# Optimization experiments

Measured on AMD Instinct MI355X. Metric: run time of the kernel, lower is better.

## Reference

```python
import jax, jax.numpy as jnp
import numpy as np

# Sampled-neighborhood sizes (NeighborSampler-style shrinking hops)
N0, N1, N2, N3 = 200000, 50000, 12500, 3200
E0, E1, E2 = 500000, 125000, 32000
D_IN, D_H, D_OUT = 128, 256, 128


def setup_inputs() -> dict:
    key = jax.random.key(0)
    ks = jax.random.split(key, 16)
    x = jax.random.normal(ks[0], (N0, D_IN), dtype=jnp.float32)
    src0 = jax.random.randint(ks[1], (E0,), 0, N0)
    dst0 = jax.random.randint(ks[2], (E0,), 0, N1)
    src1 = jax.random.randint(ks[3], (E1,), 0, N1)
    dst1 = jax.random.randint(ks[4], (E1,), 0, N2)
    src2 = jax.random.randint(ks[5], (E2,), 0, N2)
    dst2 = jax.random.randint(ks[6], (E2,), 0, N3)
    s = 0.05
    # SAGEConv params: lin_l (applied to aggregated neighbors, has bias), lin_r (root)
    wl0 = jax.random.normal(ks[7], (D_H, D_IN), dtype=jnp.float32) * s
    wr0 = jax.random.normal(ks[8], (D_H, D_IN), dtype=jnp.float32) * s
    b0 = jnp.zeros((D_H,), dtype=jnp.float32)
    wl1 = jax.random.normal(ks[9], (D_H, D_H), dtype=jnp.float32) * s
    wr1 = jax.random.normal(ks[10], (D_H, D_H), dtype=jnp.float32) * s
    b1 = jnp.zeros((D_H,), dtype=jnp.float32)
    wl2 = jax.random.normal(ks[11], (D_OUT, D_H), dtype=jnp.float32) * s
    wr2 = jax.random.normal(ks[12], (D_OUT, D_H), dtype=jnp.float32) * s
    b2 = jnp.zeros((D_OUT,), dtype=jnp.float32)
    return {"x": x, "src0": src0, "dst0": dst0, "src1": src1, "dst1": dst1,
            "src2": src2, "dst2": dst2,
            "wl0": wl0, "wr0": wr0, "b0": b0,
            "wl1": wl1, "wr1": wr1, "b1": b1,
            "wl2": wl2, "wr2": wr2, "b2": b2}


def _sage(x, src, dst, n_tgt, wl, wr, b):
    """Bipartite SAGEConv with mean aggregation (PyG default)."""
    x_tgt = x[:n_tgt]                                   # [n_tgt, d_in]
    msg = x[src]                                        # [E, d_in] gather
    s = jax.ops.segment_sum(msg, dst, num_segments=n_tgt)
    cnt = jax.ops.segment_sum(jnp.ones((src.shape[0], 1), x.dtype), dst,
                              num_segments=n_tgt)
    mean = s / jnp.maximum(cnt, 1.0)                    # mean over in-neighbors
    return mean @ wl.T + b + x_tgt @ wr.T               # [n_tgt, d_out]


def reference(x, src0, dst0, src1, dst1, src2, dst2,
              wl0, wr0, b0, wl1, wr1, b1, wl2, wr2, b2):
    h = jax.nn.relu(_sage(x, src0, dst0, N1, wl0, wr0, b0))
    h = jax.nn.relu(_sage(h, src1, dst1, N2, wl1, wr1, b1))
    return _sage(h, src2, dst2, N3, wl2, wr2, b2)       # [N3, D_OUT]
```

## Files before the change

### kernel.cpp

```cpp
#include <hip/hip_runtime.h>

#define N0s 200000
#define N1s 50000
#define N2s 12500
#define N3s 3200
#define E0s 500000
#define E1s 125000
#define E2s 32000
#define D_INs 128
#define D_Hs 256
#define D_OUTs 128

#define CAP 64
#define LOGCAP 6

#define GSTRIDE 72
#define CSTRIDE 132

#define XN4 (N0s * D_INs / 4)
#define WN4 65536
#define CAST_TOTAL (XN4 + WN4)
#define CAST_BLOCKS ((CAST_TOTAL + 2047) / 2048)

typedef __attribute__((ext_vector_type(8))) short short8;
typedef __attribute__((ext_vector_type(4))) float floatx4;

__device__ __forceinline__ unsigned short f32_to_bf16_rne(float f) {
    unsigned int u = __float_as_uint(f);
    u += 0x7fffu + ((u >> 16) & 1u);
    return (unsigned short)(u >> 16);
}
__device__ __forceinline__ float bf16_to_f32(unsigned short h) {
    return __uint_as_float(((unsigned int)h) << 16);
}

struct CastArgs {
    const float* x; unsigned short* xb;
    const float* ws_[6]; unsigned short* wd[6];
};

__launch_bounds__(256)
__global__ void cast_all(CastArgs a)
{
    #pragma unroll
    for (int j = 0; j < 8; ++j) {
        int i = blockIdx.x * 2048 + j * 256 + threadIdx.x;
        if (i < XN4) {
            float4 v = *(const float4*)&a.x[(size_t)i * 4];
            ushort4 o;
            o.x = f32_to_bf16_rne(v.x);
            o.y = f32_to_bf16_rne(v.y);
            o.z = f32_to_bf16_rne(v.z);
            o.w = f32_to_bf16_rne(v.w);
            *(ushort4*)&a.xb[(size_t)i * 4] = o;
        } else if (i < CAST_TOTAL) {
            int g = i - XN4;
            int seg, base;
            if      (g < 8192)  { seg = 0; base = 0; }
            else if (g < 16384) { seg = 1; base = 8192; }
            else if (g < 32768) { seg = 2; base = 16384; }
            else if (g < 49152) { seg = 3; base = 32768; }
            else if (g < 57344) { seg = 4; base = 49152; }
            else                { seg = 5; base = 57344; }
            int k = g - base;
            float4 v = *(const float4*)&a.ws_[seg][(size_t)k * 4];
            ushort4 o;
            o.x = f32_to_bf16_rne(v.x);
            o.y = f32_to_bf16_rne(v.y);
            o.z = f32_to_bf16_rne(v.z);
            o.w = f32_to_bf16_rne(v.w);
            *(ushort4*)&a.wd[seg][(size_t)k * 4] = o;
        }
    }
}

struct Bins {
    const int *src0, *dst0, *src1, *dst1, *src2, *dst2;
    int *cnt0, *cnt1, *cnt2;
    int *eidx0, *eidx1, *eidx2;
};

__launch_bounds__(256)
__global__ void fill3(Bins b)
{
    int e = blockIdx.x * 256 + threadIdx.x;
    if (e < E0s) {
        int d = b.dst0[e];
        int p = atomicAdd(&b.cnt0[d], 1);
        if (p < CAP) b.eidx0[(d << LOGCAP) + p] = b.src0[e];
    } else if (e < E0s + E1s) {
        int i = e - E0s;
        int d = b.dst1[i];
        int p = atomicAdd(&b.cnt1[d], 1);
        if (p < CAP) b.eidx1[(d << LOGCAP) + p] = b.src1[i];
    } else if (e < E0s + E1s + E2s) {
        int i = e - E0s - E1s;
        int d = b.dst2[i];
        int p = atomicAdd(&b.cnt2[d], 1);
        if (p < CAP) b.eidx2[(d << LOGCAP) + p] = b.src2[i];
    }
}

__launch_bounds__(256)
__global__ void gather_mean(const unsigned short* __restrict__ X,
                            const int* __restrict__ eidx,
                            const int* __restrict__ cnt,
                            unsigned short* __restrict__ out,
                            int n_tgt, int D, int logTpr)
{
    int gid = blockIdx.x * 256 + threadIdx.x;
    int row = gid >> logTpr;
    if (row >= n_tgt) return;
    int c = (gid & ((1 << logTpr) - 1)) << 2;

    int deg = cnt[row];
    int e = min(deg, CAP);
    const int* bp = &eidx[row << LOGCAP];

    float a0 = 0.f, a1 = 0.f, a2 = 0.f, a3 = 0.f;
    int i = 0;
    for (; i + 2 <= e; i += 2) {
        int s0 = bp[i], s1 = bp[i + 1];
        ushort4 v0 = *(const ushort4*)&X[(size_t)s0 * D + c];
        ushort4 v1 = *(const ushort4*)&X[(size_t)s1 * D + c];
        a0 += bf16_to_f32(v0.x) + bf16_to_f32(v1.x);
        a1 += bf16_to_f32(v0.y) + bf16_to_f32(v1.y);
        a2 += bf16_to_f32(v0.z) + bf16_to_f32(v1.z);
        a3 += bf16_to_f32(v0.w) + bf16_to_f32(v1.w);
    }
    if (i < e) {
        ushort4 v0 = *(const ushort4*)&X[(size_t)bp[i] * D + c];
        a0 += bf16_to_f32(v0.x); a1 += bf16_to_f32(v0.y);
        a2 += bf16_to_f32(v0.z); a3 += bf16_to_f32(v0.w);
    }
    float inv = 1.0f / fmaxf((float)deg, 1.0f);
    ushort4 o;
    o.x = f32_to_bf16_rne(a0 * inv);
    o.y = f32_to_bf16_rne(a1 * inv);
    o.z = f32_to_bf16_rne(a2 * inv);
    o.w = f32_to_bf16_rne(a3 * inv);
    *(ushort4*)&out[(size_t)row * D + c] = o;
}

__launch_bounds__(256)
__global__ void mfma_gemm(const unsigned short* __restrict__ A1,
                          const unsigned short* __restrict__ A2,
                          const unsigned short* __restrict__ W1,
                          const unsigned short* __restrict__ W2,
                          const float* __restrict__ bias,
                          void* __restrict__ Cout,
                          int M, int N, int K1, int K2,
                          int relu, int out_bf16)
{
    __shared__ unsigned short smem[2 * 128 * GSTRIDE];
    unsigned short* As = smem;
    unsigned short* Bs = smem + 128 * GSTRIDE;

    const int tid  = threadIdx.x;
    const int wave = tid >> 6;
    const int lane = tid & 63;
    const int quad = lane >> 4;
    const int lr   = lane & 15;
    const int wm   = wave >> 1;
    const int wn   = wave & 1;
    const int row0 = blockIdx.x * 128;
    const int col0 = blockIdx.y * 128;

    floatx4 acc[4][4] = {};

    for (int seg = 0; seg < 2; ++seg) {
        const unsigned short* Ap = (seg == 0) ? A1 : A2;
        const unsigned short* Wp = (seg == 0) ? W1 : W2;
        const int K = (seg == 0) ? K1 : K2;

        for (int k0 = 0; k0 < K; k0 += 64) {
            #pragma unroll
            for (int it = 0; it < 4; ++it) {
                int sid = tid + it * 256;
                int r = sid >> 3;
                int sc = (sid & 7) << 3;
                int gr = min(row0 + r, M - 1);
                uint4 v = *(const uint4*)&Ap[(size_t)gr * K + k0 + sc];
                *(uint4*)&As[r * GSTRIDE + sc] = v;
            }
            #pragma unroll
            for (int it = 0; it < 4; ++it) {
                int sid = tid + it * 256;
                int r = sid >> 3;
                int sc = (sid & 7) << 3;
                uint4 v = *(const uint4*)&Wp[(size_t)(col0 + r) * K + k0 + sc];
                *(uint4*)&Bs[r * GSTRIDE + sc] = v;
            }
            __syncthreads();

            #pragma unroll
            for (int kh = 0; kh < 2; ++kh) {
                short8 afr[4], bfr[4];
                #pragma unroll
                for (int mt = 0; mt < 4; ++mt)
                    afr[mt] = *(const short8*)&As[(wm * 64 + mt * 16 + lr) * GSTRIDE + kh * 32 + quad * 8];
                #pragma unroll
                for (int nt = 0; nt < 4; ++nt)
                    bfr[nt] = *(const short8*)&Bs[(wn * 64 + nt * 16 + lr) * GSTRIDE + kh * 32 + quad * 8];

                #pragma unroll
                for (int mt = 0; mt < 4; ++mt)
                    #pragma unroll
                    for (int nt = 0; nt < 4; ++nt)
                        acc[mt][nt] = __builtin_amdgcn_mfma_f32_16x16x32_bf16(
                            afr[mt], bfr[nt], acc[mt][nt], 0, 0, 0);
            }
            __syncthreads();
        }
    }

    if (out_bf16) {
        unsigned short* Cs = smem;
        #pragma unroll
        for (int nt = 0; nt < 4; ++nt) {
            int col = wn * 64 + nt * 16 + lr;
            float bv = bias[col0 + col];
            #pragma unroll
            for (int mt = 0; mt < 4; ++mt) {
                #pragma unroll
                for (int reg = 0; reg < 4; ++reg) {
                    int row = wm * 64 + mt * 16 + quad * 4 + reg;
                    float v = acc[mt][nt][reg] + bv;
                    if (relu) v = fmaxf(v, 0.f);
                    Cs[row * CSTRIDE + col] = f32_to_bf16_rne(v);
                }
            }
        }
        __syncthreads();
        int r  = tid >> 1;
        int hf = tid & 1;
        int gr = row0 + r;
        if (gr < M) {
            unsigned short* Crow = (unsigned short*)Cout + (size_t)gr * N + col0 + hf * 64;
            #pragma unroll
            for (int j = 0; j < 8; ++j) {
                uint4 v = *(const uint4*)&Cs[r * CSTRIDE + hf * 64 + j * 8];
                *(uint4*)&Crow[j * 8] = v;
            }
        }
    } else {
        #pragma unroll
        for (int nt = 0; nt < 4; ++nt) {
            int gc = col0 + wn * 64 + nt * 16 + lr;
            float bv = bias[gc];
            #pragma unroll
            for (int mt = 0; mt < 4; ++mt) {
                #pragma unroll
                for (int reg = 0; reg < 4; ++reg) {
                    int gr = row0 + wm * 64 + mt * 16 + quad * 4 + reg;
                    if (gr < M) {
                        float v = acc[mt][nt][reg] + bv;
                        if (relu) v = fmaxf(v, 0.f);
                        ((float*)Cout)[(size_t)gr * N + gc] = v;
                    }
                }
            }
        }
    }
}

extern "C" void kernel_launch(void* const* d_in, const int* in_sizes, int n_in,
                              void* d_out, int out_size, void* d_ws, size_t ws_size,
                              hipStream_t stream)
{
    const float* x   = (const float*)d_in[0];
    const int* src0  = (const int*)d_in[1];
    const int* dst0  = (const int*)d_in[2];
    const int* src1  = (const int*)d_in[3];
    const int* dst1  = (const int*)d_in[4];
    const int* src2  = (const int*)d_in[5];
    const int* dst2  = (const int*)d_in[6];
    const float* wl0 = (const float*)d_in[7];
    const float* wr0 = (const float*)d_in[8];
    const float* b0  = (const float*)d_in[9];
    const float* wl1 = (const float*)d_in[10];
    const float* wr1 = (const float*)d_in[11];
    const float* b1  = (const float*)d_in[12];
    const float* wl2 = (const float*)d_in[13];
    const float* wr2 = (const float*)d_in[14];
    const float* b2  = (const float*)d_in[15];

    unsigned short* ws = (unsigned short*)d_ws;
    unsigned short* xb    = ws;
    unsigned short* h1    = xb + (size_t)N0s * D_INs;
    unsigned short* h2    = h1 + (size_t)N1s * D_Hs;
    unsigned short* meanA = h2 + (size_t)N2s * D_Hs;
    unsigned short* wl0b  = meanA + (size_t)N1s * D_INs;
    unsigned short* wr0b  = wl0b + 32768;
    unsigned short* wl1b  = wr0b + 32768;
    unsigned short* wr1b  = wl1b + 65536;
    unsigned short* wl2b  = wr1b + 65536;
    unsigned short* wr2b  = wl2b + 32768;
    int* ib = (int*)(wr2b + 32768);
    int* cnt0 = ib;
    int* cnt1 = cnt0 + 50048;
    int* cnt2 = cnt1 + 12544;
    int* eidx0 = cnt2 + 3264;
    int* eidx1 = eidx0 + (size_t)N1s * CAP;
    int* eidx2 = eidx1 + (size_t)N2s * CAP;

    Bins b;
    b.src0 = src0; b.dst0 = dst0; b.src1 = src1; b.dst1 = dst1;
    b.src2 = src2; b.dst2 = dst2;
    b.cnt0 = cnt0; b.cnt1 = cnt1; b.cnt2 = cnt2;
    b.eidx0 = eidx0; b.eidx1 = eidx1; b.eidx2 = eidx2;

    hipMemsetAsync(cnt0, 0, (50048 + 12544 + 3264) * sizeof(int), stream);
    const int Etot = E0s + E1s + E2s;
    fill3<<<(Etot + 255) / 256, 256, 0, stream>>>(b);

    CastArgs ca;
    ca.x = x; ca.xb = xb;
    ca.ws_[0] = wl0; ca.ws_[1] = wr0; ca.ws_[2] = wl1;
    ca.ws_[3] = wr1; ca.ws_[4] = wl2; ca.ws_[5] = wr2;
    ca.wd[0] = wl0b; ca.wd[1] = wr0b; ca.wd[2] = wl1b;
    ca.wd[3] = wr1b; ca.wd[4] = wl2b; ca.wd[5] = wr2b;
    cast_all<<<CAST_BLOCKS, 256, 0, stream>>>(ca);

    {
        int th = N1s * 32;
        gather_mean<<<(th + 255) / 256, 256, 0, stream>>>(xb, eidx0, cnt0,
                                                          meanA, N1s, D_INs, 5);
        dim3 g((N1s + 127) / 128, D_Hs / 128);
        mfma_gemm<<<g, 256, 0, stream>>>(meanA, xb, wl0b, wr0b, b0, h1,
                                         N1s, D_Hs, D_INs, D_INs, 1, 1);
    }
    {
        int th = N2s * 64;
        gather_mean<<<(th + 255) / 256, 256, 0, stream>>>(h1, eidx1, cnt1,
                                                          meanA, N2s, D_Hs, 6);
        dim3 g((N2s + 127) / 128, D_Hs / 128);
        mfma_gemm<<<g, 256, 0, stream>>>(meanA, h1, wl1b, wr1b, b1, h2,
                                         N2s, D_Hs, D_Hs, D_Hs, 1, 1);
    }
    {
        int th = N3s * 64;
        gather_mean<<<(th + 255) / 256, 256, 0, stream>>>(h2, eidx2, cnt2,
                                                          meanA, N3s, D_Hs, 6);
        dim3 g((N3s + 127) / 128, D_OUTs / 128);
        mfma_gemm<<<g, 256, 0, stream>>>(meanA, h2, wl2b, wr2b, b2, (float*)d_out,
                                         N3s, D_OUTs, D_Hs, D_Hs, 0, 0);
    }
}
```

Measured before the change: 347.9 us.

## Merge prep kernels, widen gather vectors, use smaller GEMM tiles for small layers

Merges the edge-binning and bf16 cast kernels into one launch, removing a kernel boundary. The gather-mean kernel now loads 8 bf16 per thread with a 4-way unrolled neighbor loop and int4 index loads, which raises memory-level parallelism but halves the thread count. The GEMM is templated on tile size, so layers 2 and 3 use 64x64 tiles to launch more blocks on the small M. Relu and output type become compile-time parameters.

```diff
diff --git a/kernel.cpp b/kernel.cpp
--- a/kernel.cpp
+++ b/kernel.cpp
@@ -15,14 +15,15 @@
 #define LOGCAP 6
 
 #define GSTRIDE 72
-#define CSTRIDE 132
 
 #define XN4 (N0s * D_INs / 4)
 #define WN4 65536
 #define CAST_TOTAL (XN4 + WN4)
 #define CAST_BLOCKS ((CAST_TOTAL + 2047) / 2048)
+#define FILL_BLOCKS ((E0s + E1s + E2s + 255) / 256)
 
 typedef __attribute__((ext_vector_type(8))) short short8;
+typedef __attribute__((ext_vector_type(8))) unsigned short ushort8;
 typedef __attribute__((ext_vector_type(4))) float floatx4;
 
 __device__ __forceinline__ unsigned short f32_to_bf16_rne(float f) {
@@ -34,17 +35,40 @@
     return __uint_as_float(((unsigned int)h) << 16);
 }
 
-struct CastArgs {
+struct PrepArgs {
     const float* x; unsigned short* xb;
     const float* ws_[6]; unsigned short* wd[6];
+    const int *src0, *dst0, *src1, *dst1, *src2, *dst2;
+    int *cnt0, *cnt1, *cnt2;
+    int *eidx0, *eidx1, *eidx2;
 };
 
 __launch_bounds__(256)
-__global__ void cast_all(CastArgs a)
+__global__ void prep(PrepArgs a)
 {
+    if (blockIdx.x < FILL_BLOCKS) {
+        int e = blockIdx.x * 256 + threadIdx.x;
+        if (e < E0s) {
+            int d = a.dst0[e];
+            int p = atomicAdd(&a.cnt0[d], 1);
+            if (p < CAP) a.eidx0[(d << LOGCAP) + p] = a.src0[e];
+        } else if (e < E0s + E1s) {
+            int i = e - E0s;
+            int d = a.dst1[i];
+            int p = atomicAdd(&a.cnt1[d], 1);
+            if (p < CAP) a.eidx1[(d << LOGCAP) + p] = a.src1[i];
+        } else if (e < E0s + E1s + E2s) {
+            int i = e - E0s - E1s;
+            int d = a.dst2[i];
+            int p = atomicAdd(&a.cnt2[d], 1);
+            if (p < CAP) a.eidx2[(d << LOGCAP) + p] = a.src2[i];
+        }
+        return;
+    }
+    int cb = blockIdx.x - FILL_BLOCKS;
     #pragma unroll
     for (int j = 0; j < 8; ++j) {
-        int i = blockIdx.x * 2048 + j * 256 + threadIdx.x;
+        int i = cb * 2048 + j * 256 + threadIdx.x;
         if (i < XN4) {
             float4 v = *(const float4*)&a.x[(size_t)i * 4];
             ushort4 o;
@@ -74,87 +98,69 @@
     }
 }
 
-struct Bins {
-    const int *src0, *dst0, *src1, *dst1, *src2, *dst2;
-    int *cnt0, *cnt1, *cnt2;
-    int *eidx0, *eidx1, *eidx2;
-};
-
-__launch_bounds__(256)
-__global__ void fill3(Bins b)
-{
-    int e = blockIdx.x * 256 + threadIdx.x;
-    if (e < E0s) {
-        int d = b.dst0[e];
-        int p = atomicAdd(&b.cnt0[d], 1);
-        if (p < CAP) b.eidx0[(d << LOGCAP) + p] = b.src0[e];
-    } else if (e < E0s + E1s) {
-        int i = e - E0s;
-        int d = b.dst1[i];
-        int p = atomicAdd(&b.cnt1[d], 1);
-        if (p < CAP) b.eidx1[(d << LOGCAP) + p] = b.src1[i];
-    } else if (e < E0s + E1s + E2s) {
-        int i = e - E0s - E1s;
-        int d = b.dst2[i];
-        int p = atomicAdd(&b.cnt2[d], 1);
-        if (p < CAP) b.eidx2[(d << LOGCAP) + p] = b.src2[i];
-    }
-}
-
 __launch_bounds__(256)
 __global__ void gather_mean(const unsigned short* __restrict__ X,
                             const int* __restrict__ eidx,
                             const int* __restrict__ cnt,
                             unsigned short* __restrict__ out,
-                            int n_tgt, int D, int logTpr)
+                            int n_tgt, int D, int shift)
 {
     int gid = blockIdx.x * 256 + threadIdx.x;
-    int row = gid >> logTpr;
+    int row = gid >> shift;
     if (row >= n_tgt) return;
-    int c = (gid & ((1 << logTpr) - 1)) << 2;
+    int c = (gid & ((1 << shift) - 1)) << 3;
 
     int deg = cnt[row];
     int e = min(deg, CAP);
     const int* bp = &eidx[row << LOGCAP];
 
-    float a0 = 0.f, a1 = 0.f, a2 = 0.f, a3 = 0.f;
+    float acc[8];
+    #pragma unroll
+    for (int j = 0; j < 8; ++j) acc[j] = 0.f;
+
     int i = 0;
-    for (; i + 2 <= e; i += 2) {
-        int s0 = bp[i], s1 = bp[i + 1];
-        ushort4 v0 = *(const ushort4*)&X[(size_t)s0 * D + c];
-        ushort4 v1 = *(const ushort4*)&X[(size_t)s1 * D + c];
-        a0 += bf16_to_f32(v0.x) + bf16_to_f32(v1.x);
-        a1 += bf16_to_f32(v0.y) + bf16_to_f32(v1.y);
-        a2 += bf16_to_f32(v0.z) + bf16_to_f32(v1.z);
-        a3 += bf16_to_f32(v0.w) + bf16_to_f32(v1.w);
-    }
-    if (i < e) {
-        ushort4 v0 = *(const ushort4*)&X[(size_t)bp[i] * D + c];
-        a0 += bf16_to_f32(v0.x); a1 += bf16_to_f32(v0.y);
-        a2 += bf16_to_f32(v0.z); a3 += bf16_to_f32(v0.w);
-    }
+    for (; i + 4 <= e; i += 4) {
+        int4 ss = *(const int4*)&bp[i];
+        ushort8 v0 = *(const ushort8*)&X[(size_t)ss.x * D + c];
+        ushort8 v1 = *(const ushort8*)&X[(size_t)ss.y * D + c];
+        ushort8 v2 = *(const ushort8*)&X[(size_t)ss.z * D + c];
+        ushort8 v3 = *(const ushort8*)&X[(size_t)ss.w * D + c];
+        #pragma unroll
+        for (int j = 0; j < 8; ++j)
+            acc[j] += (bf16_to_f32(v0[j]) + bf16_to_f32(v1[j]))
+                    + (bf16_to_f32(v2[j]) + bf16_to_f32(v3[j]));
+    }
+    for (; i < e; ++i) {
+        ushort8 v0 = *(const ushort8*)&X[(size_t)bp[i] * D + c];
+        #pragma unroll
+        for (int j = 0; j < 8; ++j) acc[j] += bf16_to_f32(v0[j]);
+    }
+
     float inv = 1.0f / fmaxf((float)deg, 1.0f);
-    ushort4 o;
-    o.x = f32_to_bf16_rne(a0 * inv);
-    o.y = f32_to_bf16_rne(a1 * inv);
-    o.z = f32_to_bf16_rne(a2 * inv);
-    o.w = f32_to_bf16_rne(a3 * inv);
-    *(ushort4*)&out[(size_t)row * D + c] = o;
-}
-
+    ushort8 o;
+    #pragma unroll
+    for (int j = 0; j < 8; ++j) o[j] = f32_to_bf16_rne(acc[j] * inv);
+    *(ushort8*)&out[(size_t)row * D + c] = o;
+}
+
+template<int BM, int BN, int OUT_BF16, int RELU>
 __launch_bounds__(256)
-__global__ void mfma_gemm(const unsigned short* __restrict__ A1,
-                          const unsigned short* __restrict__ A2,
-                          const unsigned short* __restrict__ W1,
-                          const unsigned short* __restrict__ W2,
-                          const float* __restrict__ bias,
-                          void* __restrict__ Cout,
-                          int M, int N, int K1, int K2,
-                          int relu, int out_bf16)
+__global__ void mfma_gemm_t(const unsigned short* __restrict__ A1,
+                            const unsigned short* __restrict__ A2,
+                            const unsigned short* __restrict__ W1,
+                            const unsigned short* __restrict__ W2,
+                            const float* __restrict__ bias,
+                            void* __restrict__ Cout,
+                            int M, int N, int K1, int K2)
 {
-    __shared__ unsigned short smem[2 * 128 * GSTRIDE];
+    constexpr int MT = BM / 32;
+    constexpr int NT = BN / 32;
+    constexpr int AITER = BM / 32;
+    constexpr int CS = BN + 4;
+
+    __shared__ unsigned short smem[2 * BM * GSTRIDE];
     unsigned short* As = smem;
-    unsigned short* Bs = smem + 128 * GSTRIDE;
+    unsigned short* Bs = smem + BM * GSTRIDE;
 
     const int tid  = threadIdx.x;
     const int wave = tid >> 6;
@@ -163,10 +169,10 @@
     const int lr   = lane & 15;
     const int wm   = wave >> 1;
     const int wn   = wave & 1;
-    const int row0 = blockIdx.x * 128;
-    const int col0 = blockIdx.y * 128;
-
-    floatx4 acc[4][4] = {};
+    const int row0 = blockIdx.x * BM;
+    const int col0 = blockIdx.y * BN;
+
+    floatx4 acc[MT][NT] = {};
 
     for (int seg = 0; seg < 2; ++seg) {
         const unsigned short* Ap = (seg == 0) ? A1 : A2;
@@ -175,7 +181,7 @@
 
         for (int k0 = 0; k0 < K; k0 += 64) {
             #pragma unroll
-            for (int it = 0; it < 4; ++it) {
+            for (int it = 0; it < AITER; ++it) {
                 int sid = tid + it * 256;
                 int r = sid >> 3;
                 int sc = (sid & 7) << 3;
@@ -184,7 +190,7 @@
                 *(uint4*)&As[r * GSTRIDE + sc] = v;
             }
             #pragma unroll
-            for (int it = 0; it < 4; ++it) {
+            for (int it = 0; it < AITER; ++it) {
                 int sid = tid + it * 256;
                 int r = sid >> 3;
                 int sc = (sid & 7) << 3;
@@ -195,18 +201,18 @@
 
             #pragma unroll
             for (int kh = 0; kh < 2; ++kh) {
-                short8 afr[4], bfr[4];
-                #pragma unroll
-                for (int mt = 0; mt < 4; ++mt)
-                    afr[mt] = *(const short8*)&As[(wm * 64 + mt * 16 + lr) * GSTRIDE + kh * 32 + quad * 8];
-                #pragma unroll
-                for (int nt = 0; nt < 4; ++nt)
-                    bfr[nt] = *(const short8*)&Bs[(wn * 64 + nt * 16 + lr) * GSTRIDE + kh * 32 + quad * 8];
-
-                #pragma unroll
-                for (int mt = 0; mt < 4; ++mt)
+                short8 afr[MT], bfr[NT];
+                #pragma unroll
+                for (int mt = 0; mt < MT; ++mt)
+                    afr[mt] = *(const short8*)&As[(wm * (BM/2) + mt * 16 + lr) * GSTRIDE + kh * 32 + quad * 8];
+                #pragma unroll
+                for (int nt = 0; nt < NT; ++nt)
+                    bfr[nt] = *(const short8*)&Bs[(wn * (BN/2) + nt * 16 + lr) * GSTRIDE + kh * 32 + quad * 8];
+
+                #pragma unroll
+                for (int mt = 0; mt < MT; ++mt)
                     #pragma unroll
-                    for (int nt = 0; nt < 4; ++nt)
+                    for (int nt = 0; nt < NT; ++nt)
                         acc[mt][nt] = __builtin_amdgcn_mfma_f32_16x16x32_bf16(
                             afr[mt], bfr[nt], acc[mt][nt], 0, 0, 0);
             }
@@ -214,48 +220,50 @@
         }
     }
 
-    if (out_bf16) {
+    if (OUT_BF16) {
         unsigned short* Cs = smem;
         #pragma unroll
-        for (int nt = 0; nt < 4; ++nt) {
-            int col = wn * 64 + nt * 16 + lr;
+        for (int nt = 0; nt < NT; ++nt) {
+            int col = wn * (BN/2) + nt * 16 + lr;
             float bv = bias[col0 + col];
             #pragma unroll
-            for (int mt = 0; mt < 4; ++mt) {
+            for (int mt = 0; mt < MT; ++mt) {
                 #pragma unroll
                 for (int reg = 0; reg < 4; ++reg) {
-                    int row = wm * 64 + mt * 16 + quad * 4 + reg;
+                    int row = wm * (BM/2) + mt * 16 + quad * 4 + reg;
                     float v = acc[mt][nt][reg] + bv;
-                    if (relu) v = fmaxf(v, 0.f);
-                    Cs[row * CSTRIDE + col] = f32_to_bf16_rne(v);
+                    if (RELU) v = fmaxf(v, 0.f);
+                    Cs[row * CS + col] = f32_to_bf16_rne(v);
                 }
             }
         }
         __syncthreads();
-        int r  = tid >> 1;
-        int hf = tid & 1;
+        constexpr int TPRO = 256 / BM;
+        constexpr int SPT  = BN / TPRO;
+        int r  = tid / TPRO;
+        int hf = tid % TPRO;
         int gr = row0 + r;
         if (gr < M) {
-            unsigned short* Crow = (unsigned short*)Cout + (size_t)gr * N + col0 + hf * 64;
-            #pragma unroll
-            for (int j = 0; j < 8; ++j) {
-                uint4 v = *(const uint4*)&Cs[r * CSTRIDE + hf * 64 + j * 8];
+            unsigned short* Crow = (unsigned short*)Cout + (size_t)gr * N + col0 + hf * SPT;
+            #pragma unroll
+            for (int j = 0; j < SPT / 8; ++j) {
+                uint4 v = *(const uint4*)&Cs[r * CS + hf * SPT + j * 8];
                 *(uint4*)&Crow[j * 8] = v;
             }
         }
     } else {
         #pragma unroll
-        for (int nt = 0; nt < 4; ++nt) {
-            int gc = col0 + wn * 64 + nt * 16 + lr;
+        for (int nt = 0; nt < NT; ++nt) {
+            int gc = col0 + wn * (BN/2) + nt * 16 + lr;
             float bv = bias[gc];
             #pragma unroll
-            for (int mt = 0; mt < 4; ++mt) {
+            for (int mt = 0; mt < MT; ++mt) {
                 #pragma unroll
                 for (int reg = 0; reg < 4; ++reg) {
-                    int gr = row0 + wm * 64 + mt * 16 + quad * 4 + reg;
+                    int gr = row0 + wm * (BM/2) + mt * 16 + quad * 4 + reg;
                     if (gr < M) {
                         float v = acc[mt][nt][reg] + bv;
-                        if (relu) v = fmaxf(v, 0.f);
+                        if (RELU) v = fmaxf(v, 0.f);
                         ((float*)Cout)[(size_t)gr * N + gc] = v;
                     }
                 }
@@ -304,46 +312,42 @@
     int* eidx1 = eidx0 + (size_t)N1s * CAP;
     int* eidx2 = eidx1 + (size_t)N2s * CAP;
 
-    Bins b;
-    b.src0 = src0; b.dst0 = dst0; b.src1 = src1; b.dst1 = dst1;
-    b.src2 = src2; b.dst2 = dst2;
-    b.cnt0 = cnt0; b.cnt1 = cnt1; b.cnt2 = cnt2;
-    b.eidx0 = eidx0; b.eidx1 = eidx1; b.eidx2 = eidx2;
+    PrepArgs pa;
+    pa.x = x; pa.xb = xb;
+    pa.ws_[0] = wl0; pa.ws_[1] = wr0; pa.ws_[2] = wl1;
+    pa.ws_[3] = wr1; pa.ws_[4] = wl2; pa.ws_[5] = wr2;
+    pa.wd[0] = wl0b; pa.wd[1] = wr0b; pa.wd[2] = wl1b;
+    pa.wd[3] = wr1b; pa.wd[4] = wl2b; pa.wd[5] = wr2b;
+    pa.src0 = src0; pa.dst0 = dst0; pa.src1 = src1; pa.dst1 = dst1;
+    pa.src2 = src2; pa.dst2 = dst2;
+    pa.cnt0 = cnt0; pa.cnt1 = cnt1; pa.cnt2 = cnt2;
+    pa.eidx0 = eidx0; pa.eidx1 = eidx1; pa.eidx2 = eidx2;
 
     hipMemsetAsync(cnt0, 0, (50048 + 12544 + 3264) * sizeof(int), stream);
-    const int Etot = E0s + E1s + E2s;
-    fill3<<<(Etot + 255) / 256, 256, 0, stream>>>(b);
-
-    CastArgs ca;
-    ca.x = x; ca.xb = xb;
-    ca.ws_[0] = wl0; ca.ws_[1] = wr0; ca.ws_[2] = wl1;
-    ca.ws_[3] = wr1; ca.ws_[4] = wl2; ca.ws_[5] = wr2;
-    ca.wd[0] = wl0b; ca.wd[1] = wr0b; ca.wd[2] = wl1b;
-    ca.wd[3] = wr1b; ca.wd[4] = wl2b; ca.wd[5] = wr2b;
-    cast_all<<<CAST_BLOCKS, 256, 0, stream>>>(ca);
+    prep<<<FILL_BLOCKS + CAST_BLOCKS, 256, 0, stream>>>(pa);
 
     {
-        int th = N1s * 32;
+        int th = N1s * 16;
         gather_mean<<<(th + 255) / 256, 256, 0, stream>>>(xb, eidx0, cnt0,
-                                                          meanA, N1s, D_INs, 5);
+                                                          meanA, N1s, D_INs, 4);
         dim3 g((N1s + 127) / 128, D_Hs / 128);
-        mfma_gemm<<<g, 256, 0, stream>>>(meanA, xb, wl0b, wr0b, b0, h1,
-                                         N1s, D_Hs, D_INs, D_INs, 1, 1);
+        mfma_gemm_t<128,128,1,1><<<g, 256, 0, stream>>>(meanA, xb, wl0b, wr0b, b0, h1,
+                                                        N1s, D_Hs, D_INs, D_INs);
     }
     {
-        int th = N2s * 64;
+        int th = N2s * 32;
         gather_mean<<<(th + 255) / 256, 256, 0, stream>>>(h1, eidx1, cnt1,
-                                                          meanA, N2s, D_Hs, 6);
-        dim3 g((N2s + 127) / 128, D_Hs / 128);
-        mfma_gemm<<<g, 256, 0, stream>>>(meanA, h1, wl1b, wr1b, b1, h2,
-                                         N2s, D_Hs, D_Hs, D_Hs, 1, 1);
+                                                          meanA, N2s, D_Hs, 5);
+        dim3 g((N2s + 63) / 64, D_Hs / 64);
+        mfma_gemm_t<64,64,1,1><<<g, 256, 0, stream>>>(meanA, h1, wl1b, wr1b, b1, h2,
+                                                      N2s, D_Hs, D_Hs, D_Hs);
     }
     {
-        int th = N3s * 64;
+        int th = N3s * 32;
         gather_mean<<<(th + 255) / 256, 256, 0, stream>>>(h2, eidx2, cnt2,
-                                                          meanA, N3s, D_Hs, 6);
-        dim3 g((N3s + 127) / 128, D_OUTs / 128);
-        mfma_gemm<<<g, 256, 0, stream>>>(meanA, h2, wl2b, wr2b, b2, (float*)d_out,
-                                         N3s, D_OUTs, D_Hs, D_Hs, 0, 0);
-    }
-}
+                                                          meanA, N3s, D_Hs, 5);
+        dim3 g((N3s + 63) / 64, D_OUTs / 64);
+        mfma_gemm_t<64,64,0,0><<<g, 256, 0, stream>>>(meanA, h2, wl2b, wr2b, b2, (float*)d_out,
+                                                      N3s, D_OUTs, D_Hs, D_Hs);
+    }
+}
```

Result: faster. 318.3 us (-8.5%).
